# Kernel tuning notes

Hardware: AMD Instinct MI355X
Metric: run time of the kernel (lower is better)

The kernel has to match this reference:

```python
import jax, jax.numpy as jnp
import numpy as np

B, N, C, H, TR = 2, 5000, 256, 8, 2
M = N // TR  # reduced KV length from Conv1d(data_len, data_len//tr, 1)
DK = C // H


def setup_inputs() -> dict:
    key = jax.random.key(0)
    ks = jax.random.split(key, 10)
    s = 0.02
    return {
        "x": jax.random.normal(ks[0], (B, N, C), jnp.float32),
        "Wq": jax.random.normal(ks[1], (C, C), jnp.float32) * s,
        "bq": jnp.zeros((C,), jnp.float32),
        "Wk": jax.random.normal(ks[2], (C, C), jnp.float32) * s,
        "bk": jnp.zeros((C,), jnp.float32),
        "Wv": jax.random.normal(ks[3], (C, C), jnp.float32) * s,
        "bv": jnp.zeros((C,), jnp.float32),
        "Wc": jax.random.normal(ks[4], (M, N), jnp.float32) * (1.0 / np.sqrt(N)),
        "bc": jnp.zeros((M,), jnp.float32),
        "gamma": jnp.ones((C,), jnp.float32),
        "beta": jnp.zeros((C,), jnp.float32),
    }


def _layernorm(x, gamma, beta, eps=1e-5):
    mu = jnp.mean(x, axis=-1, keepdims=True)
    var = jnp.mean(jnp.square(x - mu), axis=-1, keepdims=True)
    return gamma * (x - mu) * jax.lax.rsqrt(var + eps) + beta


def reference(x, Wq, bq, Wk, bk, Wv, bv, Wc, bc, gamma, beta):
    b, n, c = x.shape
    # Q projection: (B, H, N, DK)
    q = (x @ Wq.T + bq).reshape(b, n, H, DK).transpose(0, 2, 1, 3)
    # Spatial reduction: Conv1d with kernel size 1 over the N (channel) dim,
    # then LayerNorm over feature dim C
    x_ = jnp.einsum('mn,bnc->bmc', Wc, x) + bc[None, :, None]
    x_ = _layernorm(x_, gamma, beta)
    k = (x_ @ Wk.T + bk).reshape(b, -1, H, DK).transpose(0, 2, 1, 3)  # (B,H,M,DK)
    v = (x_ @ Wv.T + bv).reshape(b, -1, H, DK).transpose(0, 2, 1, 3)  # (B,H,M,DK)
    # Naive attention (full score matrix, as in the original module)
    scores = jnp.einsum('bhnd,bhmd->bhnm', q, k) / jnp.sqrt(jnp.asarray(DK, x.dtype))
    p = jax.nn.softmax(scores, axis=-1)
    out = jnp.einsum('bhnm,bhmd->bhnd', p, v)
    # note: output_linear is declared in __init__ but never applied in forward
    return out.transpose(0, 2, 1, 3).reshape(b, n, c)
```

## Files before the change

kernel.cpp:

```cpp
#include <hip/hip_runtime.h>
#include <hip/hip_bf16.h>
#include <hip/hip_fp16.h>
#include <math.h>

constexpr int B = 2;
constexpr int N = 5000;
constexpr int C = 256;
constexpr int H = 8;
constexpr int DK = 32;
constexpr int M = 2500;
constexpr int MP = 2512;
constexpr int KSTEPS = 157;
constexpr int SPLIT = 8;
constexpr int MTILES = 79;
constexpr float SCALE = 0.17677669529663687f;

typedef __attribute__((ext_vector_type(8))) short bf16x8;
typedef __attribute__((ext_vector_type(4))) float f32x4;

static __device__ __forceinline__ ushort f2bf(float f) {
  __hip_bfloat16 h = __float2bfloat16(f);
  return *reinterpret_cast<ushort*>(&h);
}

__global__ __launch_bounds__(256) void wcast(const float* __restrict__ Wq,
                                             const float* __restrict__ Wk,
                                             const float* __restrict__ Wv,
                                             ushort* __restrict__ W16) {
  const float* src = (blockIdx.y == 0) ? Wq : (blockIdx.y == 1) ? Wk : Wv;
  const int idx = blockIdx.x * 1024 + threadIdx.x * 4;
  const float4 v = *reinterpret_cast<const float4*>(src + idx);
  ushort4 o;
  o.x = f2bf(v.x); o.y = f2bf(v.y); o.z = f2bf(v.z); o.w = f2bf(v.w);
  *reinterpret_cast<ushort4*>(W16 + (size_t)blockIdx.y * C * C + idx) = o;
}

__global__ __launch_bounds__(256) void xt_cast(const float* __restrict__ x,
                                               ushort* __restrict__ xTt,
                                               ushort* __restrict__ xb16) {
  const int n0 = blockIdx.x * 64, c0 = blockIdx.y * 64, b = blockIdx.z;
  const int tid = threadIdx.x;
  __shared__ ushort T[64][68];
  const float* xb = x + (size_t)b * N * C;
#pragma unroll
  for (int i = 0; i < 4; ++i) {
    const int nl = (tid >> 4) + i * 16;
    const int cg = (tid & 15) * 4;
    float4 v = {0.f, 0.f, 0.f, 0.f};
    const bool ok = (n0 + nl) < N;
    if (ok) v = *reinterpret_cast<const float4*>(xb + (size_t)(n0 + nl) * C + c0 + cg);
    ushort4 u;
    u.x = f2bf(v.x); u.y = f2bf(v.y); u.z = f2bf(v.z); u.w = f2bf(v.w);
    T[nl][cg + 0] = u.x; T[nl][cg + 1] = u.y; T[nl][cg + 2] = u.z; T[nl][cg + 3] = u.w;
    if (ok)
      *reinterpret_cast<ushort4*>(xb16 + ((size_t)b * N + n0 + nl) * C + c0 + cg) = u;
  }
  __syncthreads();
  ushort* ob = xTt + (size_t)b * KSTEPS * C * 32;
  const int cl = tid & 63, ng = tid >> 6;
#pragma unroll
  for (int j = 0; j < 2; ++j) {
    const int nstart = ng * 16 + j * 8;
    const int n = n0 + nstart;
    if (n >= KSTEPS * 32) continue;
    const int ks = n >> 5, kk = n & 31;
    ushort vals[8];
#pragma unroll
    for (int jj = 0; jj < 8; ++jj) vals[jj] = T[nstart + jj][cl];
    *reinterpret_cast<bf16x8*>(ob + ((size_t)ks * C + (c0 + cl)) * 32 + kk) =
        *reinterpret_cast<const bf16x8*>(vals);
  }
}

__global__ __launch_bounds__(256) void conv_mfma(const float* __restrict__ Wc,
                                                 const ushort* __restrict__ xTt,
                                                 ushort* __restrict__ xpart) {
  const int s = blockIdx.x & 7;
  const int mt = blockIdx.x >> 3;
  const int m0 = mt * 32;
  const int tid = threadIdx.x, w = tid >> 6, l = tid & 63;
  const int lr = l & 15, lg = l >> 4;
  f32x4 acc[16];
#pragma unroll
  for (int i = 0; i < 16; ++i) acc[i] = (f32x4){0.f, 0.f, 0.f, 0.f};
  const int row0 = m0 + lr, row1 = m0 + 16 + lr;
  const bool ok0 = row0 < M, ok1 = row1 < M;
  const float* ap0 = Wc + (size_t)(ok0 ? row0 : 0) * N + lg * 8;
  const float* ap1 = Wc + (size_t)(ok1 ? row1 : 0) * N + lg * 8;
  const int crow = w * 64 + lr;

#pragma unroll 2
  for (int ks = s; ks < KSTEPS; ks += SPLIT) {
    const int n0 = ks * 32;
    const bool kok = (n0 + lg * 8) < N;
    bf16x8 a0 = {0, 0, 0, 0, 0, 0, 0, 0}, a1 = {0, 0, 0, 0, 0, 0, 0, 0};
    if (ok0 && kok) {
      const float4 v0 = *reinterpret_cast<const float4*>(ap0 + n0);
      const float4 v1 = *reinterpret_cast<const float4*>(ap0 + n0 + 4);
      ushort u[8];
      u[0] = f2bf(v0.x); u[1] = f2bf(v0.y); u[2] = f2bf(v0.z); u[3] = f2bf(v0.w);
      u[4] = f2bf(v1.x); u[5] = f2bf(v1.y); u[6] = f2bf(v1.z); u[7] = f2bf(v1.w);
      a0 = *reinterpret_cast<const bf16x8*>(u);
    }
    if (ok1 && kok) {
      const float4 v0 = *reinterpret_cast<const float4*>(ap1 + n0);
      const float4 v1 = *reinterpret_cast<const float4*>(ap1 + n0 + 4);
      ushort u[8];
      u[0] = f2bf(v0.x); u[1] = f2bf(v0.y); u[2] = f2bf(v0.z); u[3] = f2bf(v0.w);
      u[4] = f2bf(v1.x); u[5] = f2bf(v1.y); u[6] = f2bf(v1.z); u[7] = f2bf(v1.w);
      a1 = *reinterpret_cast<const bf16x8*>(u);
    }
    bf16x8 bf[8];
#pragma unroll
    for (int ct = 0; ct < 4; ++ct)
#pragma unroll
      for (int bb = 0; bb < 2; ++bb)
        bf[ct * 2 + bb] = *reinterpret_cast<const bf16x8*>(
            xTt + (((size_t)bb * KSTEPS + ks) * C + crow + ct * 16) * 32 + lg * 8);
#pragma unroll
    for (int ct = 0; ct < 4; ++ct)
#pragma unroll
      for (int bb = 0; bb < 2; ++bb) {
        acc[(0 * 4 + ct) * 2 + bb] =
            __builtin_amdgcn_mfma_f32_16x16x32_bf16(a0, bf[ct * 2 + bb], acc[(0 * 4 + ct) * 2 + bb], 0, 0, 0);
        acc[(1 * 4 + ct) * 2 + bb] =
            __builtin_amdgcn_mfma_f32_16x16x32_bf16(a1, bf[ct * 2 + bb], acc[(1 * 4 + ct) * 2 + bb], 0, 0, 0);
      }
  }

#pragma unroll
  for (int mf = 0; mf < 2; ++mf)
#pragma unroll
    for (int ct = 0; ct < 4; ++ct)
#pragma unroll
      for (int bb = 0; bb < 2; ++bb)
#pragma unroll
        for (int i = 0; i < 4; ++i) {
          const int m = m0 + mf * 16 + lg * 4 + i;
          if (m < M) {
            const __half hv = __float2half(acc[(mf * 4 + ct) * 2 + bb][i]);
            xpart[(((size_t)s * B + bb) * M + m) * C + w * 64 + ct * 16 + lr] =
                *reinterpret_cast<const ushort*>(&hv);
          }
        }
}

__global__ __launch_bounds__(256) void ln_kernel(const ushort* __restrict__ xp,
                                                 const float* __restrict__ bc,
                                                 const float* __restrict__ gamma,
                                                 const float* __restrict__ beta,
                                                 ushort* __restrict__ xr16) {
  const int row = blockIdx.x;
  const int tid = threadIdx.x;
  const int b = row / M, m = row - b * M;
  const size_t base = (size_t)row * C;
  float v = bc[m];
#pragma unroll
  for (int s = 0; s < SPLIT; ++s) {
    const ushort us = xp[(((size_t)s * B + b) * M + m) * C + tid];
    v += __half2float(*reinterpret_cast<const __half*>(&us));
  }
  __shared__ float red[8];
  float sum = v;
#pragma unroll
  for (int o = 32; o >= 1; o >>= 1) sum += __shfl_xor(sum, o);
  if ((tid & 63) == 0) red[tid >> 6] = sum;
  __syncthreads();
  const float mu = (red[0] + red[1] + red[2] + red[3]) * (1.f / C);
  const float d = v - mu;
  float s2 = d * d;
#pragma unroll
  for (int o = 32; o >= 1; o >>= 1) s2 += __shfl_xor(s2, o);
  if ((tid & 63) == 0) red[4 + (tid >> 6)] = s2;
  __syncthreads();
  const float var = (red[4] + red[5] + red[6] + red[7]) * (1.f / C);
  xr16[base + tid] = f2bf(gamma[tid] * d * rsqrtf(var + 1e-5f) + beta[tid]);
}

__global__ __launch_bounds__(256) void proj_all(const ushort* __restrict__ xb16,
                                                const ushort* __restrict__ xr16,
                                                const ushort* __restrict__ W16,
                                                const float* __restrict__ bq,
                                                const float* __restrict__ bk,
                                                const float* __restrict__ bv,
                                                ushort* __restrict__ qb,
                                                ushort* __restrict__ kb,
                                                ushort* __restrict__ vt) {
  const int z = blockIdx.z;
  const int R = (z == 0) ? N : M;
  const int totalRows = B * R;
  if (blockIdx.x * 64 >= totalRows) return;
  const ushort* xin = (z == 0) ? xb16 : xr16;
  const ushort* W = W16 + (size_t)z * C * C;
  const float* bias = (z == 0) ? bq : (z == 1) ? bk : bv;
  const int tid = threadIdx.x, w = tid >> 6, l = tid & 63;
  const int lr = l & 15, lg = l >> 4;
  const int r0 = blockIdx.x * 64 + w * 16;
  const int c0 = blockIdx.y * 64;
  const int arow = r0 + lr;
  const bool aok = arow < totalRows;
  f32x4 acc[4] = {{0.f,0.f,0.f,0.f},{0.f,0.f,0.f,0.f},{0.f,0.f,0.f,0.f},{0.f,0.f,0.f,0.f}};
#pragma unroll
  for (int ks = 0; ks < 8; ++ks) {
    bf16x8 af = {0, 0, 0, 0, 0, 0, 0, 0};
    if (aok) af = *reinterpret_cast<const bf16x8*>(xin + (size_t)arow * C + ks * 32 + lg * 8);
#pragma unroll
    for (int ct = 0; ct < 4; ++ct) {
      const bf16x8 bf =
          *reinterpret_cast<const bf16x8*>(W + (size_t)(c0 + ct * 16 + lr) * C + ks * 32 + lg * 8);
      acc[ct] = __builtin_amdgcn_mfma_f32_16x16x32_bf16(af, bf, acc[ct], 0, 0, 0);
    }
  }
#pragma unroll
  for (int ct = 0; ct < 4; ++ct) {
    const int c = c0 + ct * 16 + lr;
    const int h = c >> 5, d = c & 31;
    const float bi = bias[c];
#pragma unroll
    for (int i = 0; i < 4; ++i) {
      const int row = r0 + lg * 4 + i;
      if (row >= totalRows) continue;
      const int bb = (row >= R) ? 1 : 0;
      const int rr = row - bb * R;
      float val = acc[ct][i] + bi;
      if (z == 0) {
        val *= SCALE;
        qb[(((size_t)bb * H + h) * N + rr) * DK + d] = f2bf(val);
      } else if (z == 1) {
        kb[(((size_t)bb * H + h) * M + rr) * DK + d] = f2bf(val);
      } else {
        vt[(((size_t)bb * H + h) * DK + d) * MP + rr] = f2bf(val);
      }
    }
  }
}

__global__ __launch_bounds__(256) void attn3(const ushort* __restrict__ q,
                                             const ushort* __restrict__ kk,
                                             const ushort* __restrict__ vt,
                                             float* __restrict__ out) {
  const int qt = blockIdx.x, h = blockIdx.y, b = blockIdx.z;
  const int tid = threadIdx.x, w = tid >> 6, l = tid & 63;
  const int lr = l & 15, lg = l >> 4;
  const int n0 = qt * 64 + w * 16;
  __shared__ ushort Plds[4][16][72];
  const ushort* qp = q + (size_t)(b * H + h) * N * DK;
  const ushort* kp = kk + (size_t)(b * H + h) * M * DK;
  const ushort* vp = vt + (size_t)(b * H + h) * DK * MP;

  bf16x8 qf = {0, 0, 0, 0, 0, 0, 0, 0};
  if (n0 + lr < N) qf = *reinterpret_cast<const bf16x8*>(qp + (size_t)(n0 + lr) * DK + lg * 8);

  f32x4 O[2] = {{0.f, 0.f, 0.f, 0.f}, {0.f, 0.f, 0.f, 0.f}};
  float psum[4] = {0.f, 0.f, 0.f, 0.f};

  constexpr int NFULL = M / 64;
  for (int t = 0; t < NFULL; ++t) {
    const int m0 = t * 64;
    f32x4 s[4];
#pragma unroll
    for (int ct = 0; ct < 4; ++ct) {
      const bf16x8 kf =
          *reinterpret_cast<const bf16x8*>(kp + (size_t)(m0 + ct * 16 + lr) * DK + lg * 8);
      s[ct] = __builtin_amdgcn_mfma_f32_16x16x32_bf16(qf, kf, (f32x4){0.f, 0.f, 0.f, 0.f}, 0, 0, 0);
    }
#pragma unroll
    for (int ct = 0; ct < 4; ++ct) {
      float pv[4];
#pragma unroll
      for (int i = 0; i < 4; ++i) {
        pv[i] = __expf(s[ct][i]);
        psum[i] += pv[i];
      }
#pragma unroll
      for (int i = 0; i < 4; i += 2) {
        __hip_bfloat162 pk = __float22bfloat162_rn(make_float2(pv[i], pv[i + 1]));
        const ushort2 u = *reinterpret_cast<const ushort2*>(&pk);
        Plds[w][lg * 4 + i][ct * 16 + lr] = u.x;
        Plds[w][lg * 4 + i + 1][ct * 16 + lr] = u.y;
      }
    }
    const bf16x8 pa0 = *reinterpret_cast<const bf16x8*>(&Plds[w][lr][lg * 8]);
    const bf16x8 pa1 = *reinterpret_cast<const bf16x8*>(&Plds[w][lr][32 + lg * 8]);
#pragma unroll
    for (int dt = 0; dt < 2; ++dt) {
      const ushort* vb = vp + (size_t)(dt * 16 + lr) * MP + m0 + lg * 8;
      const bf16x8 vf0 = *reinterpret_cast<const bf16x8*>(vb);
      const bf16x8 vf1 = *reinterpret_cast<const bf16x8*>(vb + 32);
      O[dt] = __builtin_amdgcn_mfma_f32_16x16x32_bf16(pa0, vf0, O[dt], 0, 0, 0);
      O[dt] = __builtin_amdgcn_mfma_f32_16x16x32_bf16(pa1, vf1, O[dt], 0, 0, 0);
    }
  }
  {
    const int m0 = NFULL * 64;
    f32x4 s[4];
#pragma unroll
    for (int ct = 0; ct < 4; ++ct) {
      const int mr = m0 + ct * 16 + lr;
      bf16x8 kf = {0, 0, 0, 0, 0, 0, 0, 0};
      if (mr < M) kf = *reinterpret_cast<const bf16x8*>(kp + (size_t)mr * DK + lg * 8);
      s[ct] = __builtin_amdgcn_mfma_f32_16x16x32_bf16(qf, kf, (f32x4){0.f, 0.f, 0.f, 0.f}, 0, 0, 0);
    }
#pragma unroll
    for (int ct = 0; ct < 4; ++ct) {
      const bool valid = (m0 + ct * 16 + lr) < M;
      float pv[4];
#pragma unroll
      for (int i = 0; i < 4; ++i) {
        pv[i] = valid ? __expf(s[ct][i]) : 0.f;
        psum[i] += pv[i];
      }
#pragma unroll
      for (int i = 0; i < 4; i += 2) {
        __hip_bfloat162 pk = __float22bfloat162_rn(make_float2(pv[i], pv[i + 1]));
        const ushort2 u = *reinterpret_cast<const ushort2*>(&pk);
        Plds[w][lg * 4 + i][ct * 16 + lr] = u.x;
        Plds[w][lg * 4 + i + 1][ct * 16 + lr] = u.y;
      }
    }
    const bf16x8 pa0 = *reinterpret_cast<const bf16x8*>(&Plds[w][lr][lg * 8]);
    const bf16x8 pa1 = *reinterpret_cast<const bf16x8*>(&Plds[w][lr][32 + lg * 8]);
#pragma unroll
    for (int dt = 0; dt < 2; ++dt) {
      const ushort* vb = vp + (size_t)(dt * 16 + lr) * MP + m0 + lg * 8;
      const bf16x8 vf0 = *reinterpret_cast<const bf16x8*>(vb);
      const bf16x8 vf1 = *reinterpret_cast<const bf16x8*>(vb + 32);
      O[dt] = __builtin_amdgcn_mfma_f32_16x16x32_bf16(pa0, vf0, O[dt], 0, 0, 0);
      O[dt] = __builtin_amdgcn_mfma_f32_16x16x32_bf16(pa1, vf1, O[dt], 0, 0, 0);
    }
  }
  float inv[4];
#pragma unroll
  for (int i = 0; i < 4; ++i) {
    float s2 = psum[i];
    s2 += __shfl_xor(s2, 1);
    s2 += __shfl_xor(s2, 2);
    s2 += __shfl_xor(s2, 4);
    s2 += __shfl_xor(s2, 8);
    inv[i] = 1.f / s2;
  }
#pragma unroll
  for (int i = 0; i < 4; ++i) {
    const int rq = n0 + lg * 4 + i;
    if (rq >= N) continue;
    float* ob = out + ((size_t)b * N + rq) * C + h * DK + lr;
    ob[0] = O[0][i] * inv[i];
    ob[16] = O[1][i] * inv[i];
  }
}

extern "C" void kernel_launch(void* const* d_in, const int* in_sizes, int n_in,
                              void* d_out, int out_size, void* d_ws, size_t ws_size,
                              hipStream_t stream) {
  (void)in_sizes; (void)n_in; (void)out_size; (void)ws_size;
  const float* x     = (const float*)d_in[0];
  const float* Wq    = (const float*)d_in[1];
  const float* bq    = (const float*)d_in[2];
  const float* Wk    = (const float*)d_in[3];
  const float* bk    = (const float*)d_in[4];
  const float* Wv    = (const float*)d_in[5];
  const float* bv    = (const float*)d_in[6];
  const float* Wc    = (const float*)d_in[7];
  const float* bc    = (const float*)d_in[8];
  const float* gamma = (const float*)d_in[9];
  const float* beta  = (const float*)d_in[10];
  float* out = (float*)d_out;

  char* wsb = (char*)d_ws;
  ushort* xpart = (ushort*)wsb;
  ushort* qb = (ushort*)wsb;
  ushort* kb = (ushort*)(wsb + 5120000);
  ushort* vt = (ushort*)(wsb + 7680000);
  char* p = wsb + 20480000;
  ushort* xTt  = (ushort*)p;
  ushort* xr16 = (ushort*)p;
  p += 5144576;
  ushort* xb16 = (ushort*)p; p += 5120000;
  ushort* W16  = (ushort*)p;

  wcast<<<dim3(64, 3), 256, 0, stream>>>(Wq, Wk, Wv, W16);
  xt_cast<<<dim3((N + 63) / 64, C / 64, B), 256, 0, stream>>>(x, xTt, xb16);
  conv_mfma<<<dim3(MTILES * SPLIT), 256, 0, stream>>>(Wc, xTt, xpart);
  ln_kernel<<<dim3(B * M), 256, 0, stream>>>(xpart, bc, gamma, beta, xr16);
  hipMemsetAsync(vt, 0, (size_t)B * H * DK * MP * 2, stream);
  proj_all<<<dim3((B * N + 63) / 64, C / 64, 3), 256, 0, stream>>>(xb16, xr16, W16, bq, bk, bv,
                                                                   qb, kb, vt);
  attn3<<<dim3((N + 63) / 64, H, B), 256, 0, stream>>>(qb, kb, vt, out);
}
```

Baseline: 199.8 us.

## Split attention KV range across two blocks and combine partial sums

The attention kernel now splits the KV range into two halves, each handled by a separate block that writes unnormalized partial outputs and row sums, and a new combine kernel adds the halves and normalizes. This doubles the grid to fill more compute units. The same change folds log2(e) into the Q scale to use a native exp2, swaps the MFMA operand order so P is written to LDS as packed 8-byte stores, and prefetches the next K tile in software. In exchange it adds an extra kernel launch plus a float32 round trip of a partial output buffer through global memory.

```diff
diff --git a/kernel.cpp b/kernel.cpp
--- a/kernel.cpp
+++ b/kernel.cpp
@@ -14,6 +14,7 @@
 constexpr int SPLIT = 8;
 constexpr int MTILES = 79;
 constexpr float SCALE = 0.17677669529663687f;
+constexpr float QSCALE = 0.2550598692503365f;
 
 typedef __attribute__((ext_vector_type(8))) short bf16x8;
 typedef __attribute__((ext_vector_type(4))) float f32x4;
@@ -21,6 +22,14 @@
 static __device__ __forceinline__ ushort f2bf(float f) {
   __hip_bfloat16 h = __float2bfloat16(f);
   return *reinterpret_cast<ushort*>(&h);
+}
+
+static __device__ __forceinline__ float fastexp2(float x) {
+#if __has_builtin(__builtin_amdgcn_exp2f)
+  return __builtin_amdgcn_exp2f(x);
+#else
+  return exp2f(x);
+#endif
 }
 
 __global__ __launch_bounds__(256) void wcast(const float* __restrict__ Wq,
@@ -224,7 +233,7 @@
       const int rr = row - bb * R;
       float val = acc[ct][i] + bi;
       if (z == 0) {
-        val *= SCALE;
+        val *= QSCALE;
         qb[(((size_t)bb * H + h) * N + rr) * DK + d] = f2bf(val);
       } else if (z == 1) {
         kb[(((size_t)bb * H + h) * M + rr) * DK + d] = f2bf(val);
@@ -235,11 +244,15 @@
   }
 }
 
-__global__ __launch_bounds__(256) void attn3(const ushort* __restrict__ q,
+__global__ __launch_bounds__(256) void attn4(const ushort* __restrict__ q,
                                              const ushort* __restrict__ kk,
                                              const ushort* __restrict__ vt,
-                                             float* __restrict__ out) {
-  const int qt = blockIdx.x, h = blockIdx.y, b = blockIdx.z;
+                                             float* __restrict__ o0,
+                                             float* __restrict__ o1,
+                                             float* __restrict__ ps0,
+                                             float* __restrict__ ps1) {
+  const int qt = blockIdx.x, h = blockIdx.y, z = blockIdx.z;
+  const int b = z >> 1, half = z & 1;
   const int tid = threadIdx.x, w = tid >> 6, l = tid & 63;
   const int lr = l & 15, lg = l >> 4;
   const int n0 = qt * 64 + w * 16;
@@ -247,106 +260,136 @@
   const ushort* qp = q + (size_t)(b * H + h) * N * DK;
   const ushort* kp = kk + (size_t)(b * H + h) * M * DK;
   const ushort* vp = vt + (size_t)(b * H + h) * DK * MP;
+  float* op = half ? o1 : o0;
+  float* ps = half ? ps1 : ps0;
 
   bf16x8 qf = {0, 0, 0, 0, 0, 0, 0, 0};
   if (n0 + lr < N) qf = *reinterpret_cast<const bf16x8*>(qp + (size_t)(n0 + lr) * DK + lg * 8);
 
   f32x4 O[2] = {{0.f, 0.f, 0.f, 0.f}, {0.f, 0.f, 0.f, 0.f}};
-  float psum[4] = {0.f, 0.f, 0.f, 0.f};
-
-  constexpr int NFULL = M / 64;
-  for (int t = 0; t < NFULL; ++t) {
+  float psum = 0.f;
+
+  const int tbeg = half ? 20 : 0;
+  const int tend = half ? 39 : 20;
+
+  bf16x8 kf[4];
+#pragma unroll
+  for (int ct = 0; ct < 4; ++ct)
+    kf[ct] = *reinterpret_cast<const bf16x8*>(kp + (size_t)(tbeg * 64 + ct * 16 + lr) * DK + lg * 8);
+
+#pragma unroll 2
+  for (int t = tbeg; t < tend; ++t) {
     const int m0 = t * 64;
+    bf16x8 vf[4];
+#pragma unroll
+    for (int dt = 0; dt < 2; ++dt) {
+      const ushort* vb = vp + (size_t)(dt * 16 + lr) * MP + m0 + lg * 8;
+      vf[dt * 2 + 0] = *reinterpret_cast<const bf16x8*>(vb);
+      vf[dt * 2 + 1] = *reinterpret_cast<const bf16x8*>(vb + 32);
+    }
+    const int tn = (t + 1 < tend) ? t + 1 : t;
+    bf16x8 kn[4];
+#pragma unroll
+    for (int ct = 0; ct < 4; ++ct)
+      kn[ct] = *reinterpret_cast<const bf16x8*>(kp + (size_t)(tn * 64 + ct * 16 + lr) * DK + lg * 8);
     f32x4 s[4];
 #pragma unroll
+    for (int ct = 0; ct < 4; ++ct)
+      s[ct] = __builtin_amdgcn_mfma_f32_16x16x32_bf16(kf[ct], qf, (f32x4){0.f, 0.f, 0.f, 0.f}, 0, 0, 0);
+#pragma unroll
     for (int ct = 0; ct < 4; ++ct) {
-      const bf16x8 kf =
-          *reinterpret_cast<const bf16x8*>(kp + (size_t)(m0 + ct * 16 + lr) * DK + lg * 8);
-      s[ct] = __builtin_amdgcn_mfma_f32_16x16x32_bf16(qf, kf, (f32x4){0.f, 0.f, 0.f, 0.f}, 0, 0, 0);
-    }
+      const float pv0 = fastexp2(s[ct][0]);
+      const float pv1 = fastexp2(s[ct][1]);
+      const float pv2 = fastexp2(s[ct][2]);
+      const float pv3 = fastexp2(s[ct][3]);
+      psum += (pv0 + pv1) + (pv2 + pv3);
+      __hip_bfloat162 p01 = __float22bfloat162_rn(make_float2(pv0, pv1));
+      __hip_bfloat162 p23 = __float22bfloat162_rn(make_float2(pv2, pv3));
+      uint2 u2;
+      u2.x = *reinterpret_cast<unsigned*>(&p01);
+      u2.y = *reinterpret_cast<unsigned*>(&p23);
+      *reinterpret_cast<uint2*>(&Plds[w][lr][ct * 16 + lg * 4]) = u2;
+    }
+    const bf16x8 pa0 = *reinterpret_cast<const bf16x8*>(&Plds[w][lr][lg * 8]);
+    const bf16x8 pa1 = *reinterpret_cast<const bf16x8*>(&Plds[w][lr][32 + lg * 8]);
+#pragma unroll
+    for (int dt = 0; dt < 2; ++dt) {
+      O[dt] = __builtin_amdgcn_mfma_f32_16x16x32_bf16(pa0, vf[dt * 2 + 0], O[dt], 0, 0, 0);
+      O[dt] = __builtin_amdgcn_mfma_f32_16x16x32_bf16(pa1, vf[dt * 2 + 1], O[dt], 0, 0, 0);
+    }
+#pragma unroll
+    for (int ct = 0; ct < 4; ++ct) kf[ct] = kn[ct];
+  }
+
+  if (half) {
+    const int m0 = 39 * 64;
+    bf16x8 vf[4];
+#pragma unroll
+    for (int dt = 0; dt < 2; ++dt) {
+      const ushort* vb = vp + (size_t)(dt * 16 + lr) * MP + m0 + lg * 8;
+      vf[dt * 2 + 0] = *reinterpret_cast<const bf16x8*>(vb);
+      vf[dt * 2 + 1] = *reinterpret_cast<const bf16x8*>(vb + 32);
+    }
+    bf16x8 kt[4];
+#pragma unroll
+    for (int ct = 0; ct < 4; ++ct) {
+      const int mr = m0 + ct * 16 + lr;
+      kt[ct] = (bf16x8){0, 0, 0, 0, 0, 0, 0, 0};
+      if (mr < M) kt[ct] = *reinterpret_cast<const bf16x8*>(kp + (size_t)mr * DK + lg * 8);
+    }
+    f32x4 s[4];
+#pragma unroll
+    for (int ct = 0; ct < 4; ++ct)
+      s[ct] = __builtin_amdgcn_mfma_f32_16x16x32_bf16(kt[ct], qf, (f32x4){0.f, 0.f, 0.f, 0.f}, 0, 0, 0);
 #pragma unroll
     for (int ct = 0; ct < 4; ++ct) {
       float pv[4];
 #pragma unroll
       for (int i = 0; i < 4; ++i) {
-        pv[i] = __expf(s[ct][i]);
-        psum[i] += pv[i];
+        const bool valid = (m0 + ct * 16 + lg * 4 + i) < M;
+        pv[i] = valid ? fastexp2(s[ct][i]) : 0.f;
+        psum += pv[i];
       }
-#pragma unroll
-      for (int i = 0; i < 4; i += 2) {
-        __hip_bfloat162 pk = __float22bfloat162_rn(make_float2(pv[i], pv[i + 1]));
-        const ushort2 u = *reinterpret_cast<const ushort2*>(&pk);
-        Plds[w][lg * 4 + i][ct * 16 + lr] = u.x;
-        Plds[w][lg * 4 + i + 1][ct * 16 + lr] = u.y;
-      }
+      __hip_bfloat162 p01 = __float22bfloat162_rn(make_float2(pv[0], pv[1]));
+      __hip_bfloat162 p23 = __float22bfloat162_rn(make_float2(pv[2], pv[3]));
+      uint2 u2;
+      u2.x = *reinterpret_cast<unsigned*>(&p01);
+      u2.y = *reinterpret_cast<unsigned*>(&p23);
+      *reinterpret_cast<uint2*>(&Plds[w][lr][ct * 16 + lg * 4]) = u2;
     }
     const bf16x8 pa0 = *reinterpret_cast<const bf16x8*>(&Plds[w][lr][lg * 8]);
     const bf16x8 pa1 = *reinterpret_cast<const bf16x8*>(&Plds[w][lr][32 + lg * 8]);
 #pragma unroll
     for (int dt = 0; dt < 2; ++dt) {
-      const ushort* vb = vp + (size_t)(dt * 16 + lr) * MP + m0 + lg * 8;
-      const bf16x8 vf0 = *reinterpret_cast<const bf16x8*>(vb);
-      const bf16x8 vf1 = *reinterpret_cast<const bf16x8*>(vb + 32);
-      O[dt] = __builtin_amdgcn_mfma_f32_16x16x32_bf16(pa0, vf0, O[dt], 0, 0, 0);
-      O[dt] = __builtin_amdgcn_mfma_f32_16x16x32_bf16(pa1, vf1, O[dt], 0, 0, 0);
-    }
-  }
-  {
-    const int m0 = NFULL * 64;
-    f32x4 s[4];
-#pragma unroll
-    for (int ct = 0; ct < 4; ++ct) {
-      const int mr = m0 + ct * 16 + lr;
-      bf16x8 kf = {0, 0, 0, 0, 0, 0, 0, 0};
-      if (mr < M) kf = *reinterpret_cast<const bf16x8*>(kp + (size_t)mr * DK + lg * 8);
-      s[ct] = __builtin_amdgcn_mfma_f32_16x16x32_bf16(qf, kf, (f32x4){0.f, 0.f, 0.f, 0.f}, 0, 0, 0);
-    }
-#pragma unroll
-    for (int ct = 0; ct < 4; ++ct) {
-      const bool valid = (m0 + ct * 16 + lr) < M;
-      float pv[4];
-#pragma unroll
-      for (int i = 0; i < 4; ++i) {
-        pv[i] = valid ? __expf(s[ct][i]) : 0.f;
-        psum[i] += pv[i];
-      }
-#pragma unroll
-      for (int i = 0; i < 4; i += 2) {
-        __hip_bfloat162 pk = __float22bfloat162_rn(make_float2(pv[i], pv[i + 1]));
-        const ushort2 u = *reinterpret_cast<const ushort2*>(&pk);
-        Plds[w][lg * 4 + i][ct * 16 + lr] = u.x;
-        Plds[w][lg * 4 + i + 1][ct * 16 + lr] = u.y;
-      }
-    }
-    const bf16x8 pa0 = *reinterpret_cast<const bf16x8*>(&Plds[w][lr][lg * 8]);
-    const bf16x8 pa1 = *reinterpret_cast<const bf16x8*>(&Plds[w][lr][32 + lg * 8]);
-#pragma unroll
-    for (int dt = 0; dt < 2; ++dt) {
-      const ushort* vb = vp + (size_t)(dt * 16 + lr) * MP + m0 + lg * 8;
-      const bf16x8 vf0 = *reinterpret_cast<const bf16x8*>(vb);
-      const bf16x8 vf1 = *reinterpret_cast<const bf16x8*>(vb + 32);
-      O[dt] = __builtin_amdgcn_mfma_f32_16x16x32_bf16(pa0, vf0, O[dt], 0, 0, 0);
-      O[dt] = __builtin_amdgcn_mfma_f32_16x16x32_bf16(pa1, vf1, O[dt], 0, 0, 0);
-    }
-  }
-  float inv[4];
-#pragma unroll
-  for (int i = 0; i < 4; ++i) {
-    float s2 = psum[i];
-    s2 += __shfl_xor(s2, 1);
-    s2 += __shfl_xor(s2, 2);
-    s2 += __shfl_xor(s2, 4);
-    s2 += __shfl_xor(s2, 8);
-    inv[i] = 1.f / s2;
-  }
+      O[dt] = __builtin_amdgcn_mfma_f32_16x16x32_bf16(pa0, vf[dt * 2 + 0], O[dt], 0, 0, 0);
+      O[dt] = __builtin_amdgcn_mfma_f32_16x16x32_bf16(pa1, vf[dt * 2 + 1], O[dt], 0, 0, 0);
+    }
+  }
+
+  psum += __shfl_xor(psum, 16);
+  psum += __shfl_xor(psum, 32);
+  if (lg == 0 && (n0 + lr) < N) ps[((size_t)b * H + h) * N + n0 + lr] = psum;
 #pragma unroll
   for (int i = 0; i < 4; ++i) {
     const int rq = n0 + lg * 4 + i;
     if (rq >= N) continue;
-    float* ob = out + ((size_t)b * N + rq) * C + h * DK + lr;
-    ob[0] = O[0][i] * inv[i];
-    ob[16] = O[1][i] * inv[i];
-  }
+    float* ob = op + ((size_t)b * N + rq) * C + h * DK + lr;
+    ob[0] = O[0][i];
+    ob[16] = O[1][i];
+  }
+}
+
+__global__ __launch_bounds__(256) void attn_combine(float* __restrict__ out,
+                                                    const float* __restrict__ o1,
+                                                    const float* __restrict__ ps0,
+                                                    const float* __restrict__ ps1) {
+  const int row = blockIdx.x;
+  const int c = threadIdx.x;
+  const int b = row / N, n = row - b * N;
+  const size_t pidx = ((size_t)b * H + (c >> 5)) * N + n;
+  const float denom = ps0[pidx] + ps1[pidx];
+  const size_t idx = (size_t)row * C + c;
+  out[idx] = (out[idx] + o1[idx]) / denom;
 }
 
 extern "C" void kernel_launch(void* const* d_in, const int* in_sizes, int n_in,
@@ -371,9 +414,12 @@
   ushort* qb = (ushort*)wsb;
   ushort* kb = (ushort*)(wsb + 5120000);
   ushort* vt = (ushort*)(wsb + 7680000);
+  float* ps0 = (float*)(wsb + 10400000);
+  float* ps1 = (float*)(wsb + 10720000);
   char* p = wsb + 20480000;
   ushort* xTt  = (ushort*)p;
   ushort* xr16 = (ushort*)p;
+  float* o1 = (float*)p;
   p += 5144576;
   ushort* xb16 = (ushort*)p; p += 5120000;
   ushort* W16  = (ushort*)p;
@@ -385,5 +431,6 @@
   hipMemsetAsync(vt, 0, (size_t)B * H * DK * MP * 2, stream);
   proj_all<<<dim3((B * N + 63) / 64, C / 64, 3), 256, 0, stream>>>(xb16, xr16, W16, bq, bk, bv,
                                                                    qb, kb, vt);
-  attn3<<<dim3((N + 63) / 64, H, B), 256, 0, stream>>>(qb, kb, vt, out);
-}
+  attn4<<<dim3((N + 63) / 64, H, B * 2), 256, 0, stream>>>(qb, kb, vt, out, o1, ps0, ps1);
+  attn_combine<<<dim3(B * N), 256, 0, stream>>>(out, o1, ps0, ps1);
+}
```

New measurement: 205.8 us. 1.03x slower.

## Keep softmax probabilities in registers via transposed S and fp16 PV MFMA

Applied to the files above, without the earlier changes.

The attention kernel now computes S transposed (K as the A operand), so each lane's exp outputs line up with the A-operand layout of a 16x16x16 fp16 MFMA. P is packed to fp16 in registers, which removes the LDS round trip for the probabilities. V is now stored as fp16, and log2(e) is folded into the Q scale so exp2 can be used. K for the next tile is prefetched one iteration ahead and the loop is unrolled by two. The trade-offs are more MFMA instructions of smaller K size, fp16 range limits on P and V (no max subtraction), and more register pressure.

```diff
diff --git a/kernel.cpp b/kernel.cpp
--- a/kernel.cpp
+++ b/kernel.cpp
@@ -13,14 +13,24 @@
 constexpr int KSTEPS = 157;
 constexpr int SPLIT = 8;
 constexpr int MTILES = 79;
-constexpr float SCALE = 0.17677669529663687f;
+constexpr float QSCALE = 0.2550598692503365f;
 
 typedef __attribute__((ext_vector_type(8))) short bf16x8;
 typedef __attribute__((ext_vector_type(4))) float f32x4;
+typedef __fp16 h16x2 __attribute__((ext_vector_type(2)));
+typedef _Float16 f16x4 __attribute__((ext_vector_type(4)));
 
 static __device__ __forceinline__ ushort f2bf(float f) {
   __hip_bfloat16 h = __float2bfloat16(f);
   return *reinterpret_cast<ushort*>(&h);
+}
+
+static __device__ __forceinline__ float fastexp2(float x) {
+#if __has_builtin(__builtin_amdgcn_exp2f)
+  return __builtin_amdgcn_exp2f(x);
+#else
+  return exp2f(x);
+#endif
 }
 
 __global__ __launch_bounds__(256) void wcast(const float* __restrict__ Wq,
@@ -224,18 +234,52 @@
       const int rr = row - bb * R;
       float val = acc[ct][i] + bi;
       if (z == 0) {
-        val *= SCALE;
+        val *= QSCALE;
         qb[(((size_t)bb * H + h) * N + rr) * DK + d] = f2bf(val);
       } else if (z == 1) {
         kb[(((size_t)bb * H + h) * M + rr) * DK + d] = f2bf(val);
       } else {
-        vt[(((size_t)bb * H + h) * DK + d) * MP + rr] = f2bf(val);
+        const __half hv = __float2half(val);
+        vt[(((size_t)bb * H + h) * DK + d) * MP + rr] = *reinterpret_cast<const ushort*>(&hv);
       }
     }
   }
 }
 
-__global__ __launch_bounds__(256) void attn3(const ushort* __restrict__ q,
+template <bool TAIL>
+static __device__ __forceinline__ void attn_tile(const bf16x8 (&kf)[4], const bf16x8& qf,
+                                                 const f16x4 (&vf)[8], f32x4 (&O)[2],
+                                                 float& psum, int lg, int mlim) {
+  f32x4 s[4];
+#pragma unroll
+  for (int ct = 0; ct < 4; ++ct)
+    s[ct] = __builtin_amdgcn_mfma_f32_16x16x32_bf16(kf[ct], qf, (f32x4){0.f, 0.f, 0.f, 0.f}, 0, 0, 0);
+#pragma unroll
+  for (int ct = 0; ct < 4; ++ct) {
+    float pv[4];
+#pragma unroll
+    for (int i = 0; i < 4; ++i) {
+      float e = fastexp2(s[ct][i]);
+      if (TAIL) {
+        if (ct * 16 + lg * 4 + i >= mlim) e = 0.f;
+      }
+      pv[i] = e;
+      psum += e;
+    }
+    union {
+      h16x2 h2[2];
+      f16x4 v;
+    } pk;
+    pk.h2[0] = __builtin_amdgcn_cvt_pkrtz(pv[0], pv[1]);
+    pk.h2[1] = __builtin_amdgcn_cvt_pkrtz(pv[2], pv[3]);
+    const f16x4 pa = pk.v;
+#pragma unroll
+    for (int dt = 0; dt < 2; ++dt)
+      O[dt] = __builtin_amdgcn_mfma_f32_16x16x16f16(pa, vf[ct * 2 + dt], O[dt], 0, 0, 0);
+  }
+}
+
+__global__ __launch_bounds__(256) void attn5(const ushort* __restrict__ q,
                                              const ushort* __restrict__ kk,
                                              const ushort* __restrict__ vt,
                                              float* __restrict__ out) {
@@ -243,109 +287,73 @@
   const int tid = threadIdx.x, w = tid >> 6, l = tid & 63;
   const int lr = l & 15, lg = l >> 4;
   const int n0 = qt * 64 + w * 16;
-  __shared__ ushort Plds[4][16][72];
   const ushort* qp = q + (size_t)(b * H + h) * N * DK;
   const ushort* kp = kk + (size_t)(b * H + h) * M * DK;
-  const ushort* vp = vt + (size_t)(b * H + h) * DK * MP;
+  const _Float16* vp = (const _Float16*)vt + (size_t)(b * H + h) * DK * MP;
 
   bf16x8 qf = {0, 0, 0, 0, 0, 0, 0, 0};
   if (n0 + lr < N) qf = *reinterpret_cast<const bf16x8*>(qp + (size_t)(n0 + lr) * DK + lg * 8);
 
   f32x4 O[2] = {{0.f, 0.f, 0.f, 0.f}, {0.f, 0.f, 0.f, 0.f}};
-  float psum[4] = {0.f, 0.f, 0.f, 0.f};
+  float psum = 0.f;
 
   constexpr int NFULL = M / 64;
+  bf16x8 kf[4];
+#pragma unroll
+  for (int ct = 0; ct < 4; ++ct)
+    kf[ct] = *reinterpret_cast<const bf16x8*>(kp + (size_t)(ct * 16 + lr) * DK + lg * 8);
+
+#pragma unroll 2
   for (int t = 0; t < NFULL; ++t) {
     const int m0 = t * 64;
-    f32x4 s[4];
-#pragma unroll
-    for (int ct = 0; ct < 4; ++ct) {
-      const bf16x8 kf =
-          *reinterpret_cast<const bf16x8*>(kp + (size_t)(m0 + ct * 16 + lr) * DK + lg * 8);
-      s[ct] = __builtin_amdgcn_mfma_f32_16x16x32_bf16(qf, kf, (f32x4){0.f, 0.f, 0.f, 0.f}, 0, 0, 0);
-    }
-#pragma unroll
-    for (int ct = 0; ct < 4; ++ct) {
-      float pv[4];
-#pragma unroll
-      for (int i = 0; i < 4; ++i) {
-        pv[i] = __expf(s[ct][i]);
-        psum[i] += pv[i];
-      }
-#pragma unroll
-      for (int i = 0; i < 4; i += 2) {
-        __hip_bfloat162 pk = __float22bfloat162_rn(make_float2(pv[i], pv[i + 1]));
-        const ushort2 u = *reinterpret_cast<const ushort2*>(&pk);
-        Plds[w][lg * 4 + i][ct * 16 + lr] = u.x;
-        Plds[w][lg * 4 + i + 1][ct * 16 + lr] = u.y;
-      }
-    }
-    const bf16x8 pa0 = *reinterpret_cast<const bf16x8*>(&Plds[w][lr][lg * 8]);
-    const bf16x8 pa1 = *reinterpret_cast<const bf16x8*>(&Plds[w][lr][32 + lg * 8]);
-#pragma unroll
-    for (int dt = 0; dt < 2; ++dt) {
-      const ushort* vb = vp + (size_t)(dt * 16 + lr) * MP + m0 + lg * 8;
-      const bf16x8 vf0 = *reinterpret_cast<const bf16x8*>(vb);
-      const bf16x8 vf1 = *reinterpret_cast<const bf16x8*>(vb + 32);
-      O[dt] = __builtin_amdgcn_mfma_f32_16x16x32_bf16(pa0, vf0, O[dt], 0, 0, 0);
-      O[dt] = __builtin_amdgcn_mfma_f32_16x16x32_bf16(pa1, vf1, O[dt], 0, 0, 0);
-    }
+    const int tn = (t + 1 < NFULL) ? t + 1 : t;
+    bf16x8 kn[4];
+#pragma unroll
+    for (int ct = 0; ct < 4; ++ct)
+      kn[ct] = *reinterpret_cast<const bf16x8*>(kp + (size_t)(tn * 64 + ct * 16 + lr) * DK + lg * 8);
+    f16x4 vf[8];
+#pragma unroll
+    for (int ct = 0; ct < 4; ++ct)
+#pragma unroll
+      for (int dt = 0; dt < 2; ++dt)
+        vf[ct * 2 + dt] = *reinterpret_cast<const f16x4*>(
+            vp + (size_t)(dt * 16 + lr) * MP + m0 + ct * 16 + lg * 4);
+    attn_tile<false>(kf, qf, vf, O, psum, lg, 0);
+#pragma unroll
+    for (int ct = 0; ct < 4; ++ct) kf[ct] = kn[ct];
   }
   {
     const int m0 = NFULL * 64;
-    f32x4 s[4];
+    bf16x8 kt[4];
 #pragma unroll
     for (int ct = 0; ct < 4; ++ct) {
       const int mr = m0 + ct * 16 + lr;
-      bf16x8 kf = {0, 0, 0, 0, 0, 0, 0, 0};
-      if (mr < M) kf = *reinterpret_cast<const bf16x8*>(kp + (size_t)mr * DK + lg * 8);
-      s[ct] = __builtin_amdgcn_mfma_f32_16x16x32_bf16(qf, kf, (f32x4){0.f, 0.f, 0.f, 0.f}, 0, 0, 0);
-    }
-#pragma unroll
-    for (int ct = 0; ct < 4; ++ct) {
-      const bool valid = (m0 + ct * 16 + lr) < M;
-      float pv[4];
-#pragma unroll
-      for (int i = 0; i < 4; ++i) {
-        pv[i] = valid ? __expf(s[ct][i]) : 0.f;
-        psum[i] += pv[i];
-      }
-#pragma unroll
-      for (int i = 0; i < 4; i += 2) {
-        __hip_bfloat162 pk = __float22bfloat162_rn(make_float2(pv[i], pv[i + 1]));
-        const ushort2 u = *reinterpret_cast<const ushort2*>(&pk);
-        Plds[w][lg * 4 + i][ct * 16 + lr] = u.x;
-        Plds[w][lg * 4 + i + 1][ct * 16 + lr] = u.y;
-      }
-    }
-    const bf16x8 pa0 = *reinterpret_cast<const bf16x8*>(&Plds[w][lr][lg * 8]);
-    const bf16x8 pa1 = *reinterpret_cast<const bf16x8*>(&Plds[w][lr][32 + lg * 8]);
-#pragma unroll
-    for (int dt = 0; dt < 2; ++dt) {
-      const ushort* vb = vp + (size_t)(dt * 16 + lr) * MP + m0 + lg * 8;
-      const bf16x8 vf0 = *reinterpret_cast<const bf16x8*>(vb);
-      const bf16x8 vf1 = *reinterpret_cast<const bf16x8*>(vb + 32);
-      O[dt] = __builtin_amdgcn_mfma_f32_16x16x32_bf16(pa0, vf0, O[dt], 0, 0, 0);
-      O[dt] = __builtin_amdgcn_mfma_f32_16x16x32_bf16(pa1, vf1, O[dt], 0, 0, 0);
-    }
-  }
-  float inv[4];
-#pragma unroll
-  for (int i = 0; i < 4; ++i) {
-    float s2 = psum[i];
-    s2 += __shfl_xor(s2, 1);
-    s2 += __shfl_xor(s2, 2);
-    s2 += __shfl_xor(s2, 4);
-    s2 += __shfl_xor(s2, 8);
-    inv[i] = 1.f / s2;
-  }
+      kt[ct] = (bf16x8){0, 0, 0, 0, 0, 0, 0, 0};
+      if (mr < M) kt[ct] = *reinterpret_cast<const bf16x8*>(kp + (size_t)mr * DK + lg * 8);
+    }
+    f16x4 vf[8];
+#pragma unroll
+    for (int ct = 0; ct < 4; ++ct)
+#pragma unroll
+      for (int dt = 0; dt < 2; ++dt)
+        vf[ct * 2 + dt] = *reinterpret_cast<const f16x4*>(
+            vp + (size_t)(dt * 16 + lr) * MP + m0 + ct * 16 + lg * 4);
+    attn_tile<true>(kt, qf, vf, O, psum, lg, M - m0);
+  }
+
+  psum += __shfl_xor(psum, 16);
+  psum += __shfl_xor(psum, 32);
+  const float inv = 1.f / psum;
+  float invq[4];
+#pragma unroll
+  for (int i = 0; i < 4; ++i) invq[i] = __shfl(inv, lg * 4 + i);
 #pragma unroll
   for (int i = 0; i < 4; ++i) {
     const int rq = n0 + lg * 4 + i;
     if (rq >= N) continue;
     float* ob = out + ((size_t)b * N + rq) * C + h * DK + lr;
-    ob[0] = O[0][i] * inv[i];
-    ob[16] = O[1][i] * inv[i];
+    ob[0] = O[0][i] * invq[i];
+    ob[16] = O[1][i] * invq[i];
   }
 }
 
@@ -382,8 +390,8 @@
   xt_cast<<<dim3((N + 63) / 64, C / 64, B), 256, 0, stream>>>(x, xTt, xb16);
   conv_mfma<<<dim3(MTILES * SPLIT), 256, 0, stream>>>(Wc, xTt, xpart);
   ln_kernel<<<dim3(B * M), 256, 0, stream>>>(xpart, bc, gamma, beta, xr16);
-  hipMemsetAsync(vt, 0, (size_t)B * H * DK * MP * 2, stream);
+  (void)hipMemsetAsync(vt, 0, (size_t)B * H * DK * MP * 2 + 4096, stream);
   proj_all<<<dim3((B * N + 63) / 64, C / 64, 3), 256, 0, stream>>>(xb16, xr16, W16, bq, bk, bv,
                                                                    qb, kb, vt);
-  attn3<<<dim3((N + 63) / 64, H, B), 256, 0, stream>>>(qb, kb, vt, out);
-}
+  attn5<<<dim3((N + 63) / 64, H, B), 256, 0, stream>>>(qb, kb, vt, out);
+}
```

New measurement: 589.6 us. +195.1%, slower.
